# Kernel optimization log

Measured on AMD Instinct MI355X. Metric: run time of the kernel, lower is better.

## Reference

```python
import jax, jax.numpy as jnp
import numpy as np

NUM_GROUPS = 32
EPS = 1e-6


def group_norm(x, gamma, beta):
    # x: [b, c, h, w]
    b, c, h, w = x.shape
    g = NUM_GROUPS
    xg = x.reshape(b, g, c // g, h, w)
    mean = jnp.mean(xg, axis=(2, 3, 4), keepdims=True)
    var = jnp.var(xg, axis=(2, 3, 4), keepdims=True)
    xg = (xg - mean) * jax.lax.rsqrt(var + EPS)
    x = xg.reshape(b, c, h, w)
    return x * gamma[None, :, None, None] + beta[None, :, None, None]


def conv1x1(x, w, bias):
    # x: [b, c_in, h, w], w: [c_out, c_in], bias: [c_out]
    return jnp.einsum('bihw,oi->bohw', x, w) + bias[None, :, None, None]


def setup_inputs() -> dict:
    key = jax.random.key(0)
    ks = jax.random.split(key, 10)
    c = 512
    b, h, w = 4, 64, 64
    scale = 1.0 / np.sqrt(c)
    inp = {
        'x': jax.random.normal(ks[0], (b, c, h, w), dtype=jnp.float32),
        'gn_gamma': jnp.ones((c,), dtype=jnp.float32),
        'gn_beta': jnp.zeros((c,), dtype=jnp.float32),
        'wq': jax.random.normal(ks[1], (c, c), dtype=jnp.float32) * scale,
        'bq': jnp.zeros((c,), dtype=jnp.float32),
        'wk': jax.random.normal(ks[2], (c, c), dtype=jnp.float32) * scale,
        'bk': jnp.zeros((c,), dtype=jnp.float32),
        'wv': jax.random.normal(ks[3], (c, c), dtype=jnp.float32) * scale,
        'bv': jnp.zeros((c,), dtype=jnp.float32),
        'wo': jax.random.normal(ks[4], (c, c), dtype=jnp.float32) * scale,
        'bo': jnp.zeros((c,), dtype=jnp.float32),
    }
    return inp


def reference(x, gn_gamma, gn_beta, wq, bq, wk, bk, wv, bv, wo, bo):
    b, c, h, w = x.shape
    h_ = group_norm(x, gn_gamma, gn_beta)
    q = conv1x1(h_, wq, bq)
    k = conv1x1(h_, wk, bk)
    v = conv1x1(h_, wv, bv)
    n = h * w
    q = q.reshape(b, c, n).transpose(0, 2, 1)  # [b, n, c]
    k = k.reshape(b, c, n)                      # [b, c, n]
    v = v.reshape(b, c, n).transpose(0, 2, 1)  # [b, n, c]
    sim = jnp.einsum('bqc,bck->bqk', q, k) * (c ** -0.5)  # [b, n, n]
    attn = jax.nn.softmax(sim, axis=-1)
    out = jnp.einsum('bqk,bkc->bqc', attn, v)  # [b, n, c]
    out = out.transpose(0, 2, 1).reshape(b, c, h, w)
    out = conv1x1(out, wo, bo)
    return x + out
```

## Files before the change

kernel.cpp:

```cpp
#include <hip/hip_runtime.h>


typedef __attribute__((ext_vector_type(8))) short bf16x8;
typedef __attribute__((ext_vector_type(4))) float f32x4;

#define MFMA16(a, b, c) __builtin_amdgcn_mfma_f32_16x16x32_bf16((a), (b), (c), 0, 0, 0)

#define B_   4
#define C_   512
#define N_   4096
#define SCALE 0.044194173824159216f
#define ESHIFT 12.0f
#define SC2   0.06376297465050853f
#define ES2   17.312340490667562f

__device__ __forceinline__ unsigned short f2bf(float f) {
    union { float f; unsigned int u; } v; v.f = f;
    unsigned int r = (v.u + 0x7fffu + ((v.u >> 16) & 1u)) >> 16;
    return (unsigned short)r;
}
__device__ __forceinline__ float bf2f(unsigned short s) {
    union { unsigned int u; float f; } v; v.u = ((unsigned int)s) << 16;
    return v.f;
}

__device__ __forceinline__ void async16(const unsigned short* g, unsigned short* l) {
    __builtin_amdgcn_global_load_lds((const __attribute__((address_space(1))) unsigned int*)g,
                                     (__attribute__((address_space(3))) unsigned int*)l,
                                     16, 0, 0);
}

__global__ __launch_bounds__(256) void gn_partial(const float* __restrict__ x,
                                                  float* __restrict__ part) {
    int blk = blockIdx.x;
    int gid = blk >> 2, qtr = blk & 3;
    const float4* base = (const float4*)(x + (size_t)gid * 65536) + qtr * 4096;
    float s = 0.f, ss = 0.f;
    for (int i = threadIdx.x; i < 4096; i += 256) {
        float4 v = base[i];
        s  += v.x + v.y + v.z + v.w;
        ss += v.x * v.x + v.y * v.y + v.z * v.z + v.w * v.w;
    }
    __shared__ float red[512];
    int t = threadIdx.x;
    red[t] = s; red[256 + t] = ss;
    __syncthreads();
    for (int st = 128; st > 0; st >>= 1) {
        if (t < st) { red[t] += red[t + st]; red[256 + t] += red[256 + t + st]; }
        __syncthreads();
    }
    if (t == 0) { part[blk] = red[0]; part[512 + blk] = red[256]; }
}

__global__ __launch_bounds__(256) void gn_apply(const float* __restrict__ x,
                                                const float* __restrict__ gamma,
                                                const float* __restrict__ beta,
                                                const float* __restrict__ part,
                                                unsigned short* __restrict__ ht) {
    __shared__ float tile[64][65];
    __shared__ float mrs[4][2];
    int j0 = blockIdx.x * 64, c0 = blockIdx.y * 64, b = blockIdx.z;
    int t = threadIdx.x;
    if (t < 4) {
        int gid = b * 32 + (c0 >> 4) + t;
        float s = 0.f, ss = 0.f;
#pragma unroll
        for (int q = 0; q < 4; ++q) { s += part[gid * 4 + q]; ss += part[512 + gid * 4 + q]; }
        float mean = s * (1.f / 65536.f);
        float var  = ss * (1.f / 65536.f) - mean * mean;
        mrs[t][0] = mean;
        mrs[t][1] = rsqrtf(var + 1e-6f);
    }
    __syncthreads();
#pragma unroll
    for (int i = 0; i < 16; ++i) {
        int lid = i * 256 + t;
        int cl = lid >> 6, jl = lid & 63;
        int c = c0 + cl;
        float v = x[((size_t)b * C_ + c) * N_ + j0 + jl];
        tile[cl][jl] = (v - mrs[cl >> 4][0]) * mrs[cl >> 4][1] * gamma[c] + beta[c];
    }
    __syncthreads();
#pragma unroll
    for (int i = 0; i < 16; ++i) {
        int lid = i * 256 + t;
        int jl = lid >> 6, cl = lid & 63;
        ht[((size_t)b * N_ + j0 + jl) * C_ + c0 + cl] = f2bf(tile[cl][jl]);
    }
}

__global__ __launch_bounds__(256) void wconv(const float* __restrict__ wq,
                                             const float* __restrict__ wk,
                                             const float* __restrict__ wv,
                                             const float* __restrict__ wo,
                                             unsigned short* __restrict__ dst) {
    size_t i = (size_t)blockIdx.x * 256 + threadIdx.x;
    int m = (int)(i >> 18);
    size_t off = i & 262143;
    const float* src = (m == 0) ? wq : (m == 1) ? wk : (m == 2) ? wv : wo;
    dst[i] = f2bf(src[off]);
}

template <typename EPI>
__device__ __forceinline__ void gemm_core(const unsigned short* __restrict__ Abase,
                                          const unsigned short* __restrict__ Bbase,
                                          size_t lda, size_t ldb, int K, EPI epi) {
    __shared__ unsigned short hl[2][128 * 64];
    __shared__ unsigned short wl[2][128 * 64];
    int t = threadIdx.x;
    int wv = t >> 6, lane = t & 63, l15 = lane & 15, quad = lane >> 4;
    int wm = wv & 1, wn = wv >> 1;
    int srow = lane >> 3;
    int sch  = ((lane & 7) ^ srow) * 8;
    int xr = l15 & 7;
    f32x4 acc[4][4] = {};
#pragma unroll
    for (int i = 0; i < 4; ++i) {
        int seg = wv * 4 + i;
        size_t row = seg * 8 + srow;
        async16(&Abase[row * lda + sch], &hl[0][seg * 512]);
        async16(&Bbase[row * ldb + sch], &wl[0][seg * 512]);
    }
    int nk = K >> 6;
    for (int k = 0; k < nk; ++k) {
        int cur = k & 1;
        __builtin_amdgcn_s_waitcnt(0x3F70);
        __syncthreads();
        if (k + 1 < nk) {
            int k0 = (k + 1) << 6;
#pragma unroll
            for (int i = 0; i < 4; ++i) {
                int seg = wv * 4 + i;
                size_t row = seg * 8 + srow;
                async16(&Abase[row * lda + k0 + sch], &hl[cur ^ 1][seg * 512]);
                async16(&Bbase[row * ldb + k0 + sch], &wl[cur ^ 1][seg * 512]);
            }
        }
#pragma unroll
        for (int kk = 0; kk < 2; ++kk) {
            int sl = (((kk << 2) + quad) ^ xr) * 8;
            bf16x8 af[4], bfr[4];
#pragma unroll
            for (int mi = 0; mi < 4; ++mi)
                af[mi] = *(const bf16x8*)&hl[cur][(wm * 64 + mi * 16 + l15) * 64 + sl];
#pragma unroll
            for (int ni = 0; ni < 4; ++ni)
                bfr[ni] = *(const bf16x8*)&wl[cur][(wn * 64 + ni * 16 + l15) * 64 + sl];
#pragma unroll
            for (int mi = 0; mi < 4; ++mi)
#pragma unroll
                for (int ni = 0; ni < 4; ++ni)
                    acc[mi][ni] = MFMA16(af[mi], bfr[ni], acc[mi][ni]);
        }
    }
    epi(acc, wm, wn, l15, quad);
}

__global__ __launch_bounds__(256) void gemm_qkv(const unsigned short* __restrict__ Ht,
                                                const unsigned short* __restrict__ Wb,
                                                const float* __restrict__ bq,
                                                const float* __restrict__ bk,
                                                const float* __restrict__ bv,
                                                unsigned short* __restrict__ Qt,
                                                unsigned short* __restrict__ Kt,
                                                unsigned short* __restrict__ Vg) {
    int b = blockIdx.z, j0 = blockIdx.x * 128;
    int ct = blockIdx.y;
    int slab = ct >> 2, co0 = (ct & 3) * 128;
    const unsigned short* A = Ht + ((size_t)b * N_ + j0) * C_;
    const unsigned short* B = Wb + (size_t)slab * C_ * C_ + (size_t)co0 * C_;
    const float* bias = (slab == 0) ? bq : (slab == 1) ? bk : bv;
    unsigned short* outqk = (slab == 0) ? Qt : Kt;
    gemm_core(A, B, C_, C_, C_,
        [&](f32x4 (&acc)[4][4], int wm, int wn, int l15, int quad) {
        if (slab < 2) {
#pragma unroll
            for (int mi = 0; mi < 4; ++mi)
#pragma unroll
                for (int ni = 0; ni < 4; ++ni)
#pragma unroll
                    for (int r = 0; r < 4; ++r) {
                        int mrow = wm * 64 + mi * 16 + quad * 4 + r;
                        int ncol = wn * 64 + ni * 16 + l15;
                        outqk[((size_t)b * N_ + j0 + mrow) * C_ + co0 + ncol] =
                            f2bf(acc[mi][ni][r] + bias[co0 + ncol]);
                    }
        } else {
#pragma unroll
            for (int mi = 0; mi < 4; ++mi)
#pragma unroll
                for (int ni = 0; ni < 4; ++ni) {
                    int ncol = wn * 64 + ni * 16 + l15;
                    float bb = bias[co0 + ncol];
                    ushort4 pk;
                    pk.x = f2bf(acc[mi][ni][0] + bb);
                    pk.y = f2bf(acc[mi][ni][1] + bb);
                    pk.z = f2bf(acc[mi][ni][2] + bb);
                    pk.w = f2bf(acc[mi][ni][3] + bb);
                    int jb = j0 + wm * 64 + mi * 16 + quad * 4;
                    *(ushort4*)&Vg[((size_t)b * C_ + co0 + ncol) * N_ + jb] = pk;
                }
        }
    });
}

__global__ __launch_bounds__(512, 4) void gemm_qk_exp(const unsigned short* __restrict__ Qt,
                                                      const unsigned short* __restrict__ Kt,
                                                      unsigned short* __restrict__ P,
                                                      float* __restrict__ psum) {
    extern __shared__ unsigned short sm[];
    int lin = blockIdx.x;
    int xcd = lin & 7;
    int i   = lin >> 3;
    int rid = xcd + 8 * (i >> 4);
    int idx = i & 15;
    int mi4 = idx & 1, ni4 = idx >> 1;
    int b   = rid >> 5;
    int rem = rid & 31;
    int rm  = rem & 7, rn = rem >> 3;
    int j0  = (rm * 2 + mi4) * 256;
    int ky  = rn * 8 + ni4;
    int kc0 = ky * 128;
    const unsigned short* A  = Qt + ((size_t)b * N_ + j0) * C_;
    const unsigned short* Bm = Kt + ((size_t)b * N_ + kc0) * C_;

    int t = threadIdx.x;
    int w = t >> 6, lane = t & 63, l15 = lane & 15, quad = lane >> 4;
    int wm = w >> 1, wn = w & 1;
    int srow = lane >> 2;
    int sch  = ((lane & 3) ^ ((lane >> 3) & 3)) * 8;
    int slotq = (quad ^ ((l15 >> 1) & 3)) * 8;

    const unsigned short* gA0 = A + ((size_t)(w * 2 + 0) * 16 + srow) * C_ + sch;
    const unsigned short* gA1 = A + ((size_t)(w * 2 + 1) * 16 + srow) * C_ + sch;
    const unsigned short* gB  = Bm + ((size_t)w * 16 + srow) * C_ + sch;

    f32x4 acc[4][4] = {};
    const int NT = 16;
    unsigned short* bA = sm;
    unsigned short* bB = sm + 12288;
    unsigned short* bC = sm + 24576;

    async16(gA0,      bA + (w * 2 + 0) * 512);
    async16(gA1,      bA + (w * 2 + 1) * 512);
    async16(gB,       bA + 8192 + w * 512);
    async16(gA0 + 32, bB + (w * 2 + 0) * 512);
    async16(gA1 + 32, bB + (w * 2 + 1) * 512);
    async16(gB  + 32, bB + 8192 + w * 512);
    gA0 += 64; gA1 += 64; gB += 64;
    __builtin_amdgcn_s_waitcnt(0x3F73);
    __builtin_amdgcn_s_barrier();

    for (int tt = 0; tt < NT; ++tt) {
        if (tt + 2 < NT) {
            async16(gA0, bC + (w * 2 + 0) * 512);
            async16(gA1, bC + (w * 2 + 1) * 512);
            async16(gB,  bC + 8192 + w * 512);
            gA0 += 32; gA1 += 32; gB += 32;
        }
        bf16x8 af[4], bfr[4];
#pragma unroll
        for (int mi = 0; mi < 4; ++mi)
            af[mi] = *(const bf16x8*)&bA[(wm * 64 + mi * 16 + l15) * 32 + slotq];
#pragma unroll
        for (int ni = 0; ni < 4; ++ni)
            bfr[ni] = *(const bf16x8*)&bA[8192 + (wn * 64 + ni * 16 + l15) * 32 + slotq];
        __builtin_amdgcn_s_setprio(1);
#pragma unroll
        for (int mi = 0; mi < 4; ++mi)
#pragma unroll
            for (int ni = 0; ni < 4; ++ni)
                acc[mi][ni] = MFMA16(af[mi], bfr[ni], acc[mi][ni]);
        __builtin_amdgcn_s_setprio(0);
        if (tt + 1 < NT) {
            if (tt + 2 < NT) __builtin_amdgcn_s_waitcnt(0x3F73);
            else             __builtin_amdgcn_s_waitcnt(0x3F70);
            __builtin_amdgcn_s_barrier();
        }
        unsigned short* tmp = bA; bA = bB; bB = bC; bC = tmp;
    }

#pragma unroll
    for (int mi = 0; mi < 4; ++mi) {
        float rs[4] = {0.f, 0.f, 0.f, 0.f};
#pragma unroll
        for (int ni = 0; ni < 4; ++ni) {
            int ncol = kc0 + wn * 64 + ni * 16 + l15;
#pragma unroll
            for (int r = 0; r < 4; ++r) {
                int mrow = j0 + wm * 64 + mi * 16 + quad * 4 + r;
                float p = exp2f(__builtin_fmaf(acc[mi][ni][r], SC2, -ES2));
                rs[r] += p;
                P[((size_t)b * N_ + mrow) * N_ + ncol] = f2bf(p);
            }
        }
#pragma unroll
        for (int r = 0; r < 4; ++r) {
            float v = rs[r];
            v += __shfl_xor(v, 1);
            v += __shfl_xor(v, 2);
            v += __shfl_xor(v, 4);
            v += __shfl_xor(v, 8);
            if (l15 == 0)
                psum[(size_t)(ky * 2 + wn) * 16384 +
                     (size_t)b * N_ + j0 + wm * 64 + mi * 16 + quad * 4 + r] = v;
        }
    }
}

__global__ __launch_bounds__(512, 2) void gemm_pv(const unsigned short* __restrict__ P,
                                                  const unsigned short* __restrict__ Vg,
                                                  const float* __restrict__ psum,
                                                  unsigned short* __restrict__ ao) {
    extern __shared__ unsigned short sm[];
    __shared__ float linv[256];
    int lin = blockIdx.x;
    int xcd = lin & 7;
    int i4  = lin >> 3;
    int ct  = i4 & 3;
    int grp = xcd + 8 * (i4 >> 2);
    int b = grp & 3, qtile = grp >> 2;
    int j0 = qtile * 256, co0 = ct * 128;
    int t = threadIdx.x;
    int w = t >> 6, lane = t & 63, l15 = lane & 15, quad = lane >> 4;
    int wm = w >> 1, wn = w & 1;
    int srow = lane >> 2;
    int sch  = ((lane & 3) ^ ((lane >> 3) & 3)) * 8;
    int slotq = (quad ^ ((l15 >> 1) & 3)) * 8;
    const unsigned short* A  = P  + ((size_t)b * N_ + j0) * N_;
    const unsigned short* Bm = Vg + ((size_t)b * C_ + co0) * N_;
    f32x4 acc[4][4] = {};
    const int NT = 128;
#pragma unroll
    for (int tt = 0; tt < 2; ++tt) {
        unsigned short* dst = sm + tt * 12288;
        size_t k0 = (size_t)tt << 5;
#pragma unroll
        for (int i = 0; i < 2; ++i) {
            int seg = w * 2 + i;
            size_t row = (size_t)seg * 16 + srow;
            async16(&A[row * N_ + k0 + sch], dst + seg * 512);
        }
        {
            size_t row = (size_t)w * 16 + srow;
            async16(&Bm[row * N_ + k0 + sch], dst + 8192 + w * 512);
        }
    }
    if (t < 256) {
        size_t q = (size_t)b * N_ + j0 + t;
        float s = 0.f;
#pragma unroll
        for (int i = 0; i < 64; ++i) s += psum[(size_t)i * 16384 + q];
        linv[t] = 1.f / s;
    }
    __builtin_amdgcn_s_waitcnt(0x3F73);
    __builtin_amdgcn_s_barrier();
    for (int tt = 0; tt < NT; tt += 2) {
#pragma unroll
        for (int s = 0; s < 2; ++s) {
            int tc = tt + s;
            const unsigned short* bp = sm + (tc & 3) * 12288;
            int ts = tc + 2;
            bf16x8 af[4], bfr[4];
#pragma unroll
            for (int mi = 0; mi < 4; ++mi)
                af[mi] = *(const bf16x8*)&bp[(wm * 64 + mi * 16 + l15) * 32 + slotq];
#pragma unroll
            for (int ni = 0; ni < 4; ++ni)
                bfr[ni] = *(const bf16x8*)&bp[8192 + (wn * 64 + ni * 16 + l15) * 32 + slotq];
            if (ts < NT) {
                unsigned short* stg = sm + (ts & 3) * 12288;
                size_t k0n = (size_t)ts << 5;
#pragma unroll
                for (int i = 0; i < 2; ++i) {
                    int seg = w * 2 + i;
                    size_t row = (size_t)seg * 16 + srow;
                    async16(&A[row * N_ + k0n + sch], stg + seg * 512);
                }
                {
                    size_t row = (size_t)w * 16 + srow;
                    async16(&Bm[row * N_ + k0n + sch], stg + 8192 + w * 512);
                }
            }
            __builtin_amdgcn_s_setprio(1);
#pragma unroll
            for (int mi = 0; mi < 4; ++mi)
#pragma unroll
                for (int ni = 0; ni < 4; ++ni)
                    acc[mi][ni] = MFMA16(af[mi], bfr[ni], acc[mi][ni]);
            __builtin_amdgcn_s_setprio(0);
            if (s == 0) {
                if (tt + 2 < NT) __builtin_amdgcn_s_waitcnt(0x3F73);
                else             __builtin_amdgcn_s_waitcnt(0x3F70);
                __builtin_amdgcn_sched_barrier(0);
            }
        }
        if (tt + 2 < NT) {
            if (tt + 3 < NT) __builtin_amdgcn_s_waitcnt(0x3F73);
            else             __builtin_amdgcn_s_waitcnt(0x3F70);
            __builtin_amdgcn_s_barrier();
        }
    }
#pragma unroll
    for (int mi = 0; mi < 4; ++mi)
#pragma unroll
        for (int ni = 0; ni < 4; ++ni)
#pragma unroll
            for (int r = 0; r < 4; ++r) {
                int mrow = wm * 64 + mi * 16 + quad * 4 + r;
                int ncol = wn * 64 + ni * 16 + l15;
                ao[((size_t)b * N_ + j0 + mrow) * C_ + co0 + ncol] =
                    f2bf(acc[mi][ni][r] * linv[mrow]);
            }
}

__global__ __launch_bounds__(256) void gemm_resid(const unsigned short* __restrict__ AObf,
                                                  const unsigned short* __restrict__ Wo,
                                                  const float* __restrict__ bo,
                                                  const float* __restrict__ xres,
                                                  float* __restrict__ out) {
    int b = blockIdx.z, j0 = blockIdx.x * 128, co0 = blockIdx.y * 128;
    const unsigned short* A = AObf + ((size_t)b * N_ + j0) * C_;
    const unsigned short* B = Wo + (size_t)co0 * C_;
    gemm_core(A, B, C_, C_, C_,
        [&](f32x4 (&acc)[4][4], int wm, int wn, int l15, int quad) {
#pragma unroll
        for (int mi = 0; mi < 4; ++mi)
#pragma unroll
            for (int ni = 0; ni < 4; ++ni) {
                int ncol = wn * 64 + ni * 16 + l15;
                int jb = j0 + wm * 64 + mi * 16 + quad * 4;
                size_t o = ((size_t)b * C_ + co0 + ncol) * N_ + jb;
                float bb = bo[co0 + ncol];
                float4 xr = *(const float4*)&xres[o];
                float4 ov;
                ov.x = acc[mi][ni][0] + bb + xr.x;
                ov.y = acc[mi][ni][1] + bb + xr.y;
                ov.z = acc[mi][ni][2] + bb + xr.z;
                ov.w = acc[mi][ni][3] + bb + xr.w;
                *(float4*)&out[o] = ov;
            }
    });
}

__global__ __launch_bounds__(256, 1) void flash_attn(const unsigned short* __restrict__ Qt,
                                                     const unsigned short* __restrict__ Kt,
                                                     const unsigned short* __restrict__ Vg,
                                                     unsigned short* __restrict__ part,
                                                     float* __restrict__ lbuf,
                                                     int nsplit) {
    extern __shared__ unsigned short smem[];
    unsigned short* Kl = smem;
    unsigned short* Vl = smem + 32768;
    unsigned short* Pl = smem + 65536;

    int flat = blockIdx.x;
    int qblk, b, s;
    if (nsplit == 2) { s = flat & 1; b = (flat >> 1) & 3; qblk = flat >> 3; }
    else             { s = 0;        b = flat & 3;        qblk = flat >> 2; }
    int q0 = qblk * 128;
    int t = threadIdx.x, w = t >> 6, lane = t & 63, l15 = lane & 15, quad = lane >> 4;
    int klen = N_ / nsplit, kbeg = s * klen, nkt = klen / 32;
    int xr = l15 & 7;

    const unsigned short* Kbase = Kt + (size_t)b * N_ * C_;
    const unsigned short* Vbase = Vg + (size_t)b * C_ * N_;

    bf16x8 qa[2][16];
#pragma unroll
    for (int u = 0; u < 2; ++u) {
        const unsigned short* qb =
            Qt + ((size_t)b * N_ + q0 + w * 32 + u * 16 + l15) * C_ + quad * 8;
#pragma unroll
        for (int ck = 0; ck < 16; ++ck) qa[u][ck] = *(const bf16x8*)(qb + ck * 32);
    }

    f32x4 o[2][32] = {};
    float lrow[2][4] = {};

    {
        int k0 = kbeg;
#pragma unroll
        for (int i = 0; i < 8; ++i) {
            int r = w * 8 + i;
            async16(Kbase + (size_t)(k0 + r) * C_ + ((lane ^ (r & 7)) * 8), Kl + r * 512);
        }
#pragma unroll
        for (int i = 0; i < 8; ++i) {
            int idx = w * 8 + i, kc = idx >> 3, cb = idx & 7;
            async16(Vbase + (size_t)(cb * 64 + lane) * N_ + k0 + kc * 8,
                    Vl + (kc * 512 + cb * 64) * 8);
        }
    }

    for (int kt = 0; kt < nkt; ++kt) {
        int cur = kt & 1, nxt = cur ^ 1;
        __builtin_amdgcn_s_waitcnt(0x3F70);
        __syncthreads();
        if (kt + 1 < nkt) {
            int k0 = kbeg + (kt + 1) * 32;
#pragma unroll
            for (int i = 0; i < 8; ++i) {
                int r = w * 8 + i;
                async16(Kbase + (size_t)(k0 + r) * C_ + ((lane ^ (r & 7)) * 8),
                        Kl + nxt * 16384 + r * 512);
            }
#pragma unroll
            for (int i = 0; i < 8; ++i) {
                int idx = w * 8 + i, kc = idx >> 3, cb = idx & 7;
                async16(Vbase + (size_t)(cb * 64 + lane) * N_ + k0 + kc * 8,
                        Vl + nxt * 16384 + (kc * 512 + cb * 64) * 8);
            }
        }
        const unsigned short* Kc = Kl + cur * 16384;
        f32x4 s00 = {}, s01 = {}, s10 = {}, s11 = {};
#pragma unroll
        for (int ck = 0; ck < 16; ++ck) {
            int slot = (ck * 4 + quad) ^ xr;
            bf16x8 b0 = *(const bf16x8*)&Kc[l15 * 512 + slot * 8];
            bf16x8 b1 = *(const bf16x8*)&Kc[(16 + l15) * 512 + slot * 8];
            s00 = MFMA16(qa[0][ck], b0, s00);
            s10 = MFMA16(qa[1][ck], b0, s10);
            s01 = MFMA16(qa[0][ck], b1, s01);
            s11 = MFMA16(qa[1][ck], b1, s11);
        }
        unsigned short* pb = &Pl[w * 1152];
#pragma unroll
        for (int r = 0; r < 4; ++r) {
            float p00 = __expf(s00[r] * SCALE - ESHIFT);
            float p01 = __expf(s01[r] * SCALE - ESHIFT);
            float p10 = __expf(s10[r] * SCALE - ESHIFT);
            float p11 = __expf(s11[r] * SCALE - ESHIFT);
            lrow[0][r] += p00 + p01;
            lrow[1][r] += p10 + p11;
            int row0 = (quad * 4 + r) * 36;
            int row1 = (16 + quad * 4 + r) * 36;
            pb[row0 + l15]      = f2bf(p00);
            pb[row0 + 16 + l15] = f2bf(p01);
            pb[row1 + l15]      = f2bf(p10);
            pb[row1 + 16 + l15] = f2bf(p11);
        }
        __builtin_amdgcn_s_waitcnt(0xC07F);
        bf16x8 pa0 = *(const bf16x8*)&Pl[w * 1152 + l15 * 36 + quad * 8];
        bf16x8 pa1 = *(const bf16x8*)&Pl[w * 1152 + (16 + l15) * 36 + quad * 8];
        const unsigned short* Vc = Vl + cur * 16384;
#pragma unroll
        for (int cf = 0; cf < 32; ++cf) {
            bf16x8 vb = *(const bf16x8*)&Vc[(quad * 512 + cf * 16 + l15) * 8];
            o[0][cf] = MFMA16(pa0, vb, o[0][cf]);
            o[1][cf] = MFMA16(pa1, vb, o[1][cf]);
        }
    }
#pragma unroll
    for (int u = 0; u < 2; ++u)
#pragma unroll
        for (int r = 0; r < 4; ++r) {
            float l = lrow[u][r];
            l += __shfl_xor(l, 1);
            l += __shfl_xor(l, 2);
            l += __shfl_xor(l, 4);
            l += __shfl_xor(l, 8);
            lrow[u][r] = l;
        }
    size_t pbase = (size_t)(s * B_ + b) * N_;
#pragma unroll
    for (int u = 0; u < 2; ++u)
#pragma unroll
        for (int cf = 0; cf < 32; ++cf)
#pragma unroll
            for (int r = 0; r < 4; ++r) {
                int q = q0 + w * 32 + u * 16 + quad * 4 + r;
                part[(pbase + q) * C_ + cf * 16 + l15] = f2bf(o[u][cf][r]);
            }
    if (l15 == 0) {
#pragma unroll
        for (int u = 0; u < 2; ++u)
#pragma unroll
            for (int r = 0; r < 4; ++r) {
                int q = q0 + w * 32 + u * 16 + quad * 4 + r;
                lbuf[pbase + q] = lrow[u][r];
            }
    }
}

__global__ __launch_bounds__(256) void attn_combine(const unsigned short* __restrict__ part,
                                                    const float* __restrict__ lbuf,
                                                    unsigned short* __restrict__ ao,
                                                    int nsplit) {
    size_t idx = (size_t)blockIdx.x * 256 + threadIdx.x;
    int cu = (int)(idx & 63);
    size_t row = idx >> 6;
    float l = lbuf[row];
    union { uint4 v; unsigned short u[8]; } p1, p2, outv;
    p1.v = *(const uint4*)&part[row * C_ + cu * 8];
    if (nsplit == 2) {
        l += lbuf[(size_t)B_ * N_ + row];
        p2.v = *(const uint4*)&part[((size_t)B_ * N_ + row) * C_ + cu * 8];
    } else {
        p2.v = make_uint4(0, 0, 0, 0);
    }
    float inv = 1.f / l;
#pragma unroll
    for (int j = 0; j < 8; ++j)
        outv.u[j] = f2bf((bf2f(p1.u[j]) + bf2f(p2.u[j])) * inv);
    *(uint4*)&ao[row * C_ + cu * 8] = outv.v;
}

extern "C" void kernel_launch(void* const* d_in, const int* in_sizes, int n_in,
                              void* d_out, int out_size, void* d_ws, size_t ws_size,
                              hipStream_t stream) {
    const float* x   = (const float*)d_in[0];
    const float* gam = (const float*)d_in[1];
    const float* bet = (const float*)d_in[2];
    const float* wq  = (const float*)d_in[3];
    const float* bq  = (const float*)d_in[4];
    const float* wk  = (const float*)d_in[5];
    const float* bk  = (const float*)d_in[6];
    const float* wv  = (const float*)d_in[7];
    const float* bv  = (const float*)d_in[8];
    const float* wo  = (const float*)d_in[9];
    const float* bo  = (const float*)d_in[10];
    float* out = (float*)d_out;

    char* ws = (char*)d_ws;
    const size_t SZH = (size_t)B_ * N_ * C_ * 2;
    const size_t OFF_HT = 4096;
    const size_t OFF_QT = OFF_HT + SZH;
    const size_t OFF_KT = OFF_QT + SZH;
    const size_t OFF_VG = OFF_KT + SZH;
    const size_t OFF_WB = OFF_VG + SZH;
    const size_t OFF_X  = OFF_WB + 2097152;
    float*          part0 = (float*)ws;
    unsigned short* Ht    = (unsigned short*)(ws + OFF_HT);
    unsigned short* Qt    = (unsigned short*)(ws + OFF_QT);
    unsigned short* Kt    = (unsigned short*)(ws + OFF_KT);
    unsigned short* Vg    = (unsigned short*)(ws + OFF_VG);
    unsigned short* Wb    = (unsigned short*)(ws + OFF_WB);
    unsigned short* AObf  = Ht;

    const size_t SZPSUM = 64ull * 16384 * 4;
    const size_t SZP    = (size_t)B_ * N_ * N_ * 2;
    float*          psum = (float*)(ws + OFF_X);
    unsigned short* P    = (unsigned short*)(ws + OFF_X + SZPSUM);
    size_t needA = OFF_X + SZPSUM + SZP;

    float*          lbuf = (float*)(ws + OFF_X);
    unsigned short* partb = (unsigned short*)(ws + OFF_X + 262144);
    size_t needB2 = OFF_X + 262144 + 2 * SZH;

    gn_partial<<<512, 256, 0, stream>>>(x, part0);
    gn_apply<<<dim3(64, 8, B_), 256, 0, stream>>>(x, gam, bet, part0, Ht);
    wconv<<<4096, 256, 0, stream>>>(wq, wk, wv, wo, Wb);
    gemm_qkv<<<dim3(32, 12, B_), 256, 0, stream>>>(Ht, Wb, bq, bk, bv, Qt, Kt, Vg);

    if (ws_size >= needA) {
        const int QK_LDS = 73728;
        (void)hipFuncSetAttribute((const void*)gemm_qk_exp,
                                  hipFuncAttributeMaxDynamicSharedMemorySize, QK_LDS);
        gemm_qk_exp<<<2048, 512, QK_LDS, stream>>>(Qt, Kt, P, psum);
        const int PV_LDS = 98304;
        (void)hipFuncSetAttribute((const void*)gemm_pv,
                                  hipFuncAttributeMaxDynamicSharedMemorySize, PV_LDS);
        gemm_pv<<<256, 512, PV_LDS, stream>>>(P, Vg, psum, AObf);
    } else {
        int nsplit = (ws_size >= needB2) ? 2 : 1;
        const int FLASH_LDS = 140288;
        (void)hipFuncSetAttribute((const void*)flash_attn,
                                  hipFuncAttributeMaxDynamicSharedMemorySize, FLASH_LDS);
        flash_attn<<<dim3(32 * B_ * nsplit), 256, FLASH_LDS, stream>>>(Qt, Kt, Vg, partb, lbuf, nsplit);
        attn_combine<<<4096, 256, 0, stream>>>(partb, lbuf, AObf, nsplit);
    }
    gemm_resid<<<dim3(32, 4, B_), 256, 0, stream>>>(AObf, Wb + 786432, bo, x, out);
}
```

Before: 320.2 us.

## Factor QK pipeline into shared core and reuse it for QKV projection

Pulls the triple-buffered 512-thread, 256x128-tile MFMA main loop out of the QK kernel into a reusable core. The QKV projection now uses this core in place of the 256-thread double-buffered 128x128 GEMM, with a 1D grid whose ordering interleaves Q/K/V slabs. It also inserts sched_barrier calls after the pipeline barriers in the QK and PV kernels to stop the compiler reordering instructions across them. The aim is better latency hiding and fewer CTAs in the projection, at the cost of higher LDS use per block and a changed epilogue mapping for the larger tile.

After: 330.3 us. 1.03x slower.

```diff
diff --git a/kernel.cpp b/kernel.cpp
--- a/kernel.cpp
+++ b/kernel.cpp
@@ -102,76 +102,89 @@
 }
 
 template <typename EPI>
-__device__ __forceinline__ void gemm_core(const unsigned short* __restrict__ Abase,
-                                          const unsigned short* __restrict__ Bbase,
-                                          size_t lda, size_t ldb, int K, EPI epi) {
-    __shared__ unsigned short hl[2][128 * 64];
-    __shared__ unsigned short wl[2][128 * 64];
+__device__ __forceinline__ void lean_core(const unsigned short* __restrict__ A,
+                                          const unsigned short* __restrict__ Bm,
+                                          size_t lda, size_t ldb, int NT,
+                                          unsigned short* sm, EPI epi) {
     int t = threadIdx.x;
-    int wv = t >> 6, lane = t & 63, l15 = lane & 15, quad = lane >> 4;
-    int wm = wv & 1, wn = wv >> 1;
-    int srow = lane >> 3;
-    int sch  = ((lane & 7) ^ srow) * 8;
-    int xr = l15 & 7;
+    int w = t >> 6, lane = t & 63, l15 = lane & 15, quad = lane >> 4;
+    int wm = w >> 1, wn = w & 1;
+    int srow = lane >> 2;
+    int sch  = ((lane & 3) ^ ((lane >> 3) & 3)) * 8;
+    int slotq = (quad ^ ((l15 >> 1) & 3)) * 8;
+
+    const unsigned short* gA0 = A + ((size_t)(w * 2 + 0) * 16 + srow) * lda + sch;
+    const unsigned short* gA1 = A + ((size_t)(w * 2 + 1) * 16 + srow) * lda + sch;
+    const unsigned short* gB  = Bm + ((size_t)w * 16 + srow) * ldb + sch;
+
     f32x4 acc[4][4] = {};
-#pragma unroll
-    for (int i = 0; i < 4; ++i) {
-        int seg = wv * 4 + i;
-        size_t row = seg * 8 + srow;
-        async16(&Abase[row * lda + sch], &hl[0][seg * 512]);
-        async16(&Bbase[row * ldb + sch], &wl[0][seg * 512]);
-    }
-    int nk = K >> 6;
-    for (int k = 0; k < nk; ++k) {
-        int cur = k & 1;
-        __builtin_amdgcn_s_waitcnt(0x3F70);
-        __syncthreads();
-        if (k + 1 < nk) {
-            int k0 = (k + 1) << 6;
-#pragma unroll
-            for (int i = 0; i < 4; ++i) {
-                int seg = wv * 4 + i;
-                size_t row = seg * 8 + srow;
-                async16(&Abase[row * lda + k0 + sch], &hl[cur ^ 1][seg * 512]);
-                async16(&Bbase[row * ldb + k0 + sch], &wl[cur ^ 1][seg * 512]);
-            }
-        }
-#pragma unroll
-        for (int kk = 0; kk < 2; ++kk) {
-            int sl = (((kk << 2) + quad) ^ xr) * 8;
-            bf16x8 af[4], bfr[4];
-#pragma unroll
-            for (int mi = 0; mi < 4; ++mi)
-                af[mi] = *(const bf16x8*)&hl[cur][(wm * 64 + mi * 16 + l15) * 64 + sl];
+    unsigned short* bA = sm;
+    unsigned short* bB = sm + 12288;
+    unsigned short* bC = sm + 24576;
+
+    async16(gA0,      bA + (w * 2 + 0) * 512);
+    async16(gA1,      bA + (w * 2 + 1) * 512);
+    async16(gB,       bA + 8192 + w * 512);
+    async16(gA0 + 32, bB + (w * 2 + 0) * 512);
+    async16(gA1 + 32, bB + (w * 2 + 1) * 512);
+    async16(gB  + 32, bB + 8192 + w * 512);
+    gA0 += 64; gA1 += 64; gB += 64;
+    __builtin_amdgcn_s_waitcnt(0x3F73);
+    __builtin_amdgcn_s_barrier();
+    __builtin_amdgcn_sched_barrier(0);
+
+    for (int tt = 0; tt < NT; ++tt) {
+        if (tt + 2 < NT) {
+            async16(gA0, bC + (w * 2 + 0) * 512);
+            async16(gA1, bC + (w * 2 + 1) * 512);
+            async16(gB,  bC + 8192 + w * 512);
+            gA0 += 32; gA1 += 32; gB += 32;
+        }
+        bf16x8 af[4], bfr[4];
+#pragma unroll
+        for (int mi = 0; mi < 4; ++mi)
+            af[mi] = *(const bf16x8*)&bA[(wm * 64 + mi * 16 + l15) * 32 + slotq];
+#pragma unroll
+        for (int ni = 0; ni < 4; ++ni)
+            bfr[ni] = *(const bf16x8*)&bA[8192 + (wn * 64 + ni * 16 + l15) * 32 + slotq];
+        __builtin_amdgcn_s_setprio(1);
+#pragma unroll
+        for (int mi = 0; mi < 4; ++mi)
 #pragma unroll
             for (int ni = 0; ni < 4; ++ni)
-                bfr[ni] = *(const bf16x8*)&wl[cur][(wn * 64 + ni * 16 + l15) * 64 + sl];
-#pragma unroll
-            for (int mi = 0; mi < 4; ++mi)
-#pragma unroll
-                for (int ni = 0; ni < 4; ++ni)
-                    acc[mi][ni] = MFMA16(af[mi], bfr[ni], acc[mi][ni]);
-        }
+                acc[mi][ni] = MFMA16(af[mi], bfr[ni], acc[mi][ni]);
+        __builtin_amdgcn_s_setprio(0);
+        if (tt + 1 < NT) {
+            if (tt + 2 < NT) __builtin_amdgcn_s_waitcnt(0x3F73);
+            else             __builtin_amdgcn_s_waitcnt(0x3F70);
+            __builtin_amdgcn_s_barrier();
+            __builtin_amdgcn_sched_barrier(0);
+        }
+        unsigned short* tmp = bA; bA = bB; bB = bC; bC = tmp;
     }
     epi(acc, wm, wn, l15, quad);
 }
 
-__global__ __launch_bounds__(256) void gemm_qkv(const unsigned short* __restrict__ Ht,
-                                                const unsigned short* __restrict__ Wb,
-                                                const float* __restrict__ bq,
-                                                const float* __restrict__ bk,
-                                                const float* __restrict__ bv,
-                                                unsigned short* __restrict__ Qt,
-                                                unsigned short* __restrict__ Kt,
-                                                unsigned short* __restrict__ Vg) {
-    int b = blockIdx.z, j0 = blockIdx.x * 128;
-    int ct = blockIdx.y;
-    int slab = ct >> 2, co0 = (ct & 3) * 128;
+__global__ __launch_bounds__(512, 4) void gemm_qkv2(const unsigned short* __restrict__ Ht,
+                                                    const unsigned short* __restrict__ Wb,
+                                                    const float* __restrict__ bq,
+                                                    const float* __restrict__ bk,
+                                                    const float* __restrict__ bv,
+                                                    unsigned short* __restrict__ Qt,
+                                                    unsigned short* __restrict__ Kt,
+                                                    unsigned short* __restrict__ Vg) {
+    extern __shared__ unsigned short sm[];
+    int lin = blockIdx.x;
+    int slab = lin % 3;
+    int q    = lin / 3;
+    int b  = q & 3;
+    int ct = (q >> 2) & 3, jt = q >> 4;
+    int j0 = jt * 256, co0 = ct * 128;
     const unsigned short* A = Ht + ((size_t)b * N_ + j0) * C_;
     const unsigned short* B = Wb + (size_t)slab * C_ * C_ + (size_t)co0 * C_;
     const float* bias = (slab == 0) ? bq : (slab == 1) ? bk : bv;
     unsigned short* outqk = (slab == 0) ? Qt : Kt;
-    gemm_core(A, B, C_, C_, C_,
+    lean_core(A, B, C_, C_, 16, sm,
         [&](f32x4 (&acc)[4][4], int wm, int wn, int l15, int quad) {
         if (slab < 2) {
 #pragma unroll
@@ -223,89 +236,35 @@
     int kc0 = ky * 128;
     const unsigned short* A  = Qt + ((size_t)b * N_ + j0) * C_;
     const unsigned short* Bm = Kt + ((size_t)b * N_ + kc0) * C_;
-
-    int t = threadIdx.x;
-    int w = t >> 6, lane = t & 63, l15 = lane & 15, quad = lane >> 4;
-    int wm = w >> 1, wn = w & 1;
-    int srow = lane >> 2;
-    int sch  = ((lane & 3) ^ ((lane >> 3) & 3)) * 8;
-    int slotq = (quad ^ ((l15 >> 1) & 3)) * 8;
-
-    const unsigned short* gA0 = A + ((size_t)(w * 2 + 0) * 16 + srow) * C_ + sch;
-    const unsigned short* gA1 = A + ((size_t)(w * 2 + 1) * 16 + srow) * C_ + sch;
-    const unsigned short* gB  = Bm + ((size_t)w * 16 + srow) * C_ + sch;
-
-    f32x4 acc[4][4] = {};
-    const int NT = 16;
-    unsigned short* bA = sm;
-    unsigned short* bB = sm + 12288;
-    unsigned short* bC = sm + 24576;
-
-    async16(gA0,      bA + (w * 2 + 0) * 512);
-    async16(gA1,      bA + (w * 2 + 1) * 512);
-    async16(gB,       bA + 8192 + w * 512);
-    async16(gA0 + 32, bB + (w * 2 + 0) * 512);
-    async16(gA1 + 32, bB + (w * 2 + 1) * 512);
-    async16(gB  + 32, bB + 8192 + w * 512);
-    gA0 += 64; gA1 += 64; gB += 64;
-    __builtin_amdgcn_s_waitcnt(0x3F73);
-    __builtin_amdgcn_s_barrier();
-
-    for (int tt = 0; tt < NT; ++tt) {
-        if (tt + 2 < NT) {
-            async16(gA0, bC + (w * 2 + 0) * 512);
-            async16(gA1, bC + (w * 2 + 1) * 512);
-            async16(gB,  bC + 8192 + w * 512);
-            gA0 += 32; gA1 += 32; gB += 32;
-        }
-        bf16x8 af[4], bfr[4];
-#pragma unroll
-        for (int mi = 0; mi < 4; ++mi)
-            af[mi] = *(const bf16x8*)&bA[(wm * 64 + mi * 16 + l15) * 32 + slotq];
-#pragma unroll
-        for (int ni = 0; ni < 4; ++ni)
-            bfr[ni] = *(const bf16x8*)&bA[8192 + (wn * 64 + ni * 16 + l15) * 32 + slotq];
-        __builtin_amdgcn_s_setprio(1);
-#pragma unroll
-        for (int mi = 0; mi < 4; ++mi)
-#pragma unroll
-            for (int ni = 0; ni < 4; ++ni)
-                acc[mi][ni] = MFMA16(af[mi], bfr[ni], acc[mi][ni]);
-        __builtin_amdgcn_s_setprio(0);
-        if (tt + 1 < NT) {
-            if (tt + 2 < NT) __builtin_amdgcn_s_waitcnt(0x3F73);
-            else             __builtin_amdgcn_s_waitcnt(0x3F70);
-            __builtin_amdgcn_s_barrier();
-        }
-        unsigned short* tmp = bA; bA = bB; bB = bC; bC = tmp;
-    }
-
-#pragma unroll
-    for (int mi = 0; mi < 4; ++mi) {
-        float rs[4] = {0.f, 0.f, 0.f, 0.f};
-#pragma unroll
-        for (int ni = 0; ni < 4; ++ni) {
-            int ncol = kc0 + wn * 64 + ni * 16 + l15;
+    lean_core(A, Bm, C_, C_, 16, sm,
+        [&](f32x4 (&acc)[4][4], int wm, int wn, int l15, int quad) {
+#pragma unroll
+        for (int mi = 0; mi < 4; ++mi) {
+            float rs[4] = {0.f, 0.f, 0.f, 0.f};
+#pragma unroll
+            for (int ni = 0; ni < 4; ++ni) {
+                int ncol = kc0 + wn * 64 + ni * 16 + l15;
+#pragma unroll
+                for (int r = 0; r < 4; ++r) {
+                    int mrow = j0 + wm * 64 + mi * 16 + quad * 4 + r;
+                    float p = exp2f(__builtin_fmaf(acc[mi][ni][r], SC2, -ES2));
+                    rs[r] += p;
+                    P[((size_t)b * N_ + mrow) * N_ + ncol] = f2bf(p);
+                }
+            }
 #pragma unroll
             for (int r = 0; r < 4; ++r) {
-                int mrow = j0 + wm * 64 + mi * 16 + quad * 4 + r;
-                float p = exp2f(__builtin_fmaf(acc[mi][ni][r], SC2, -ES2));
-                rs[r] += p;
-                P[((size_t)b * N_ + mrow) * N_ + ncol] = f2bf(p);
-            }
-        }
-#pragma unroll
-        for (int r = 0; r < 4; ++r) {
-            float v = rs[r];
-            v += __shfl_xor(v, 1);
-            v += __shfl_xor(v, 2);
-            v += __shfl_xor(v, 4);
-            v += __shfl_xor(v, 8);
-            if (l15 == 0)
-                psum[(size_t)(ky * 2 + wn) * 16384 +
-                     (size_t)b * N_ + j0 + wm * 64 + mi * 16 + quad * 4 + r] = v;
-        }
-    }
+                float v = rs[r];
+                v += __shfl_xor(v, 1);
+                v += __shfl_xor(v, 2);
+                v += __shfl_xor(v, 4);
+                v += __shfl_xor(v, 8);
+                if (l15 == 0)
+                    psum[(size_t)(ky * 2 + wn) * 16384 +
+                         (size_t)b * N_ + j0 + wm * 64 + mi * 16 + quad * 4 + r] = v;
+            }
+        }
+    });
 }
 
 __global__ __launch_bounds__(512, 2) void gemm_pv(const unsigned short* __restrict__ P,
@@ -355,6 +314,7 @@
     }
     __builtin_amdgcn_s_waitcnt(0x3F73);
     __builtin_amdgcn_s_barrier();
+    __builtin_amdgcn_sched_barrier(0);
     for (int tt = 0; tt < NT; tt += 2) {
 #pragma unroll
         for (int s = 0; s < 2; ++s) {
@@ -399,6 +359,7 @@
             if (tt + 3 < NT) __builtin_amdgcn_s_waitcnt(0x3F73);
             else             __builtin_amdgcn_s_waitcnt(0x3F70);
             __builtin_amdgcn_s_barrier();
+            __builtin_amdgcn_sched_barrier(0);
         }
     }
 #pragma unroll
@@ -412,6 +373,61 @@
                 ao[((size_t)b * N_ + j0 + mrow) * C_ + co0 + ncol] =
                     f2bf(acc[mi][ni][r] * linv[mrow]);
             }
+}
+
+template <typename EPI>
+__device__ __forceinline__ void gemm_core(const unsigned short* __restrict__ Abase,
+                                          const unsigned short* __restrict__ Bbase,
+                                          size_t lda, size_t ldb, int K, EPI epi) {
+    __shared__ unsigned short hl[2][128 * 64];
+    __shared__ unsigned short wl[2][128 * 64];
+    int t = threadIdx.x;
+    int wv = t >> 6, lane = t & 63, l15 = lane & 15, quad = lane >> 4;
+    int wm = wv & 1, wn = wv >> 1;
+    int srow = lane >> 3;
+    int sch  = ((lane & 7) ^ srow) * 8;
+    int xr = l15 & 7;
+    f32x4 acc[4][4] = {};
+#pragma unroll
+    for (int i = 0; i < 4; ++i) {
+        int seg = wv * 4 + i;
+        size_t row = seg * 8 + srow;
+        async16(&Abase[row * lda + sch], &hl[0][seg * 512]);
+        async16(&Bbase[row * ldb + sch], &wl[0][seg * 512]);
+    }
+    int nk = K >> 6;
+    for (int k = 0; k < nk; ++k) {
+        int cur = k & 1;
+        __builtin_amdgcn_s_waitcnt(0x3F70);
+        __syncthreads();
+        if (k + 1 < nk) {
+            int k0 = (k + 1) << 6;
+#pragma unroll
+            for (int i = 0; i < 4; ++i) {
+                int seg = wv * 4 + i;
+                size_t row = seg * 8 + srow;
+                async16(&Abase[row * lda + k0 + sch], &hl[cur ^ 1][seg * 512]);
+                async16(&Bbase[row * ldb + k0 + sch], &wl[cur ^ 1][seg * 512]);
+            }
+        }
+#pragma unroll
+        for (int kk = 0; kk < 2; ++kk) {
+            int sl = (((kk << 2) + quad) ^ xr) * 8;
+            bf16x8 af[4], bfr[4];
+#pragma unroll
+            for (int mi = 0; mi < 4; ++mi)
+                af[mi] = *(const bf16x8*)&hl[cur][(wm * 64 + mi * 16 + l15) * 64 + sl];
+#pragma unroll
+            for (int ni = 0; ni < 4; ++ni)
+                bfr[ni] = *(const bf16x8*)&wl[cur][(wn * 64 + ni * 16 + l15) * 64 + sl];
+#pragma unroll
+            for (int mi = 0; mi < 4; ++mi)
+#pragma unroll
+                for (int ni = 0; ni < 4; ++ni)
+                    acc[mi][ni] = MFMA16(af[mi], bfr[ni], acc[mi][ni]);
+        }
+    }
+    epi(acc, wm, wn, l15, quad);
 }
 
 __global__ __launch_bounds__(256) void gemm_resid(const unsigned short* __restrict__ AObf,
@@ -642,22 +658,25 @@
     const size_t SZP    = (size_t)B_ * N_ * N_ * 2;
     float*          psum = (float*)(ws + OFF_X);
     unsigned short* P    = (unsigned short*)(ws + OFF_X + SZPSUM);
-    size_t needA = OFF_X + SZPSUM + SZP;
+    size_t needA  = OFF_X + SZPSUM + SZP;
 
     float*          lbuf = (float*)(ws + OFF_X);
     unsigned short* partb = (unsigned short*)(ws + OFF_X + 262144);
     size_t needB2 = OFF_X + 262144 + 2 * SZH;
 
+    const int LEAN_LDS = 73728;
+
     gn_partial<<<512, 256, 0, stream>>>(x, part0);
     gn_apply<<<dim3(64, 8, B_), 256, 0, stream>>>(x, gam, bet, part0, Ht);
     wconv<<<4096, 256, 0, stream>>>(wq, wk, wv, wo, Wb);
-    gemm_qkv<<<dim3(32, 12, B_), 256, 0, stream>>>(Ht, Wb, bq, bk, bv, Qt, Kt, Vg);
+    (void)hipFuncSetAttribute((const void*)gemm_qkv2,
+                              hipFuncAttributeMaxDynamicSharedMemorySize, LEAN_LDS);
+    gemm_qkv2<<<768, 512, LEAN_LDS, stream>>>(Ht, Wb, bq, bk, bv, Qt, Kt, Vg);
 
     if (ws_size >= needA) {
-        const int QK_LDS = 73728;
         (void)hipFuncSetAttribute((const void*)gemm_qk_exp,
-                                  hipFuncAttributeMaxDynamicSharedMemorySize, QK_LDS);
-        gemm_qk_exp<<<2048, 512, QK_LDS, stream>>>(Qt, Kt, P, psum);
+                                  hipFuncAttributeMaxDynamicSharedMemorySize, LEAN_LDS);
+        gemm_qk_exp<<<2048, 512, LEAN_LDS, stream>>>(Qt, Kt, P, psum);
         const int PV_LDS = 98304;
         (void)hipFuncSetAttribute((const void*)gemm_pv,
                                   hipFuncAttributeMaxDynamicSharedMemorySize, PV_LDS);
```
